# Performance work log

Hardware: AMD Instinct MI355X
Metric: run time of the kernel (lower is better)

The kernel has to match this reference:

```python
import jax, jax.numpy as jnp
import numpy as np

POS_L, DIR_L, TIME_L = 10, 4, 4
R, S, H = 2048, 128, 256


def posenc(x, L):
    # torch order: [x, sin(f0*x), cos(f0*x), sin(f1*x), cos(f1*x), ...]
    freqs = 2.0 ** jnp.arange(L, dtype=x.dtype)          # log-sampled bands
    xf = x[..., None, :] * freqs[:, None]                # [..., L, C]
    sc = jnp.stack([jnp.sin(xf), jnp.cos(xf)], axis=-2)  # [..., L, 2, C]
    return jnp.concatenate([x, sc.reshape(*x.shape[:-1], -1)], axis=-1)


def mlp(x, params):
    *hidden, last = params
    for W, b in hidden:
        x = jax.nn.relu(x @ W + b)
    W, b = last
    return x @ W + b


def compute_weights(sigma, z_vals):
    delta = jnp.concatenate(
        [z_vals[..., 1:] - z_vals[..., :-1], jnp.full_like(z_vals[..., :1], 1e10)], axis=-1)
    alpha = 1.0 - jnp.exp(-sigma * delta)
    trans = jnp.cumprod(
        jnp.concatenate([jnp.ones_like(alpha[..., :1]), 1.0 - alpha + 1e-10], axis=-1),
        axis=-1)[..., :-1]
    return alpha * trans


def _init_mlp(kbase, dims):
    Ws, bs = [], []
    for i, (din, dout) in enumerate(zip(dims[:-1], dims[1:])):
        Ws.append(jax.random.normal(jax.random.fold_in(kbase, i), (din, dout), jnp.float32)
                  / jnp.sqrt(jnp.float32(din)))
        bs.append(jnp.zeros((dout,), jnp.float32))
    bs[-1] = bs[-1].at[0].set(1.0)  # bias sigma positive so compositing is well-behaved
    return Ws, bs


def setup_inputs() -> dict:
    key = jax.random.key(0)
    k = jax.random.split(key, 6)
    points = jax.random.normal(k[0], (R, S, 3), jnp.float32)
    dirs = jax.random.normal(k[1], (R, S, 3), jnp.float32)
    z_vals = 2.0 + 4.0 * jnp.sort(jax.random.uniform(k[2], (R, S), jnp.float32), axis=-1)
    time = jax.random.uniform(k[3], (R, S), jnp.float32)
    sdims = [90, H, H, H, H, 4]
    ddims = [99, H, H, H, H, 5]
    sW, sb = _init_mlp(k[4], sdims)
    dW, db = _init_mlp(k[5], ddims)
    inp = {"points": points, "dirs": dirs, "z_vals": z_vals, "time": time}
    for i in range(5):
        inp[f"static_W{i}"] = sW[i]
        inp[f"static_b{i}"] = sb[i]
        inp[f"dynamic_W{i}"] = dW[i]
        inp[f"dynamic_b{i}"] = db[i]
    return inp


def reference(points, dirs, z_vals, time,
              static_W0, static_b0, static_W1, static_b1, static_W2, static_b2,
              static_W3, static_b3, static_W4, static_b4,
              dynamic_W0, dynamic_b0, dynamic_W1, dynamic_b1, dynamic_W2, dynamic_b2,
              dynamic_W3, dynamic_b3, dynamic_W4, dynamic_b4):
    sparams = [(static_W0, static_b0), (static_W1, static_b1), (static_W2, static_b2),
               (static_W3, static_b3), (static_W4, static_b4)]
    dparams = [(dynamic_W0, dynamic_b0), (dynamic_W1, dynamic_b1), (dynamic_W2, dynamic_b2),
               (dynamic_W3, dynamic_b3), (dynamic_W4, dynamic_b4)]

    enc_p = posenc(points, POS_L)                 # [R,S,63]
    enc_d = posenc(dirs, DIR_L)                   # [R,S,27]
    enc_t = posenc(time[..., None], TIME_L)       # [R,S,9]

    static_out = mlp(jnp.concatenate([enc_p, enc_d], axis=-1), sparams)            # [R,S,4]
    dynamic_out = mlp(jnp.concatenate([enc_p, enc_d, enc_t], axis=-1), dparams)    # [R,S,5]

    static_sigma = static_out[..., 0]
    static_rgb = jax.nn.sigmoid(static_out[..., 1:4])
    dynamic_sigma = dynamic_out[..., 0]
    dynamic_rgb = jax.nn.sigmoid(dynamic_out[..., 1:4])
    bw = jax.nn.sigmoid(dynamic_out[..., 4])      # [R,S] blend weight

    sigma = (1.0 - bw) * static_sigma + bw * dynamic_sigma           # [R,S]
    rgb = (1.0 - bw)[..., None] * static_rgb + bw[..., None] * dynamic_rgb  # [R,S,3]

    weights = compute_weights(sigma, z_vals)                         # [R,S]
    rgb_map = jnp.sum(weights[..., None] * rgb, axis=-2)             # [R,3]
    depth_map = jnp.sum(weights * z_vals, axis=-1)                   # [R]
    static_weights = (1.0 - bw) * weights
    dynamic_weights = bw * weights
    return rgb_map, depth_map, weights, static_weights, dynamic_weights
```

## Files before the change

### kernel.cpp

```cpp
#include <hip/hip_runtime.h>
#include <math.h>


#define RAYS 2048
#define SAMP 128
#define MTOT (RAYS * SAMP)
#define HD   256
#define BM   128
#define ES   136
#define HS   264

#define OUT_RGB   0
#define OUT_DEPTH 6144
#define OUT_W     8192
#define OUT_SW    270336
#define OUT_DW    532480

#define SW0 0
#define SW1 32768
#define SW2 98304
#define SW3 163840
#define SW4 229376
#define DW0 233472
#define DW1 266240
#define DW2 331776
#define DW3 397312
#define DW4 462848
#define WTOT 466944

typedef __attribute__((ext_vector_type(8))) short short8;
typedef __attribute__((ext_vector_type(4))) float f32x4;
typedef __attribute__((ext_vector_type(2))) float f32x2;
typedef __attribute__((ext_vector_type(2))) unsigned int uint2v;

__device__ __forceinline__ float sigm(float x) { return 1.0f / (1.0f + expf(-x)); }

__device__ __forceinline__ short f2bf(float f) {
    union { float f; unsigned u; } v; v.f = f;
    unsigned r = v.u + 0x7fffu + ((v.u >> 16) & 1u);
    return (short)(r >> 16);
}

#define GLB_LOAD(dst, ptr, imm) \
    asm volatile("global_load_dwordx4 %0, %1, off offset:%c2" \
                 : "=v"(dst) : "v"(ptr), "n"(imm))
#define LDS_READ(dst, addr, imm) \
    asm volatile("ds_read_b128 %0, %1 offset:%c2" \
                 : "=v"(dst) : "v"(addr), "n"(imm))
#define WAITCNT(vm, lg) do { \
    asm volatile("s_waitcnt vmcnt(%c0) lgkmcnt(%c1)" :: "n"(vm), "n"(lg)); \
    __builtin_amdgcn_sched_barrier(0); } while (0)

__device__ __forceinline__ void bar_lgkm() {
    __builtin_amdgcn_sched_barrier(0);
    asm volatile("s_waitcnt lgkmcnt(0)\n\ts_barrier" ::: "memory");
    __builtin_amdgcn_sched_barrier(0);
}
__device__ __forceinline__ void bar_only() {
    __builtin_amdgcn_sched_barrier(0);
    asm volatile("s_barrier" ::: "memory");
    __builtin_amdgcn_sched_barrier(0);
}

__device__ __forceinline__ void conv1(const float* __restrict__ src, short* __restrict__ dst,
                                      int local, int K, int N, int Kpad) {
    const int n = local / Kpad, k = local - n * Kpad;
    const float v = (k < K && n < N) ? src[k * N + n] : 0.0f;
    dst[local] = f2bf(v);
}

__global__ __launch_bounds__(256)
void prep_weights(const float* sW0, const float* sW1, const float* sW2,
                  const float* sW3, const float* sW4,
                  const float* dW0, const float* dW1, const float* dW2,
                  const float* dW3, const float* dW4, short* __restrict__ dst)
{
    const int idx = blockIdx.x * 256 + threadIdx.x;
    if (idx >= WTOT) return;
    if      (idx < SW1) conv1(sW0, dst + SW0, idx - SW0,  90, 256, 128);
    else if (idx < SW2) conv1(sW1, dst + SW1, idx - SW1, 256, 256, 256);
    else if (idx < SW3) conv1(sW2, dst + SW2, idx - SW2, 256, 256, 256);
    else if (idx < SW4) conv1(sW3, dst + SW3, idx - SW3, 256, 256, 256);
    else if (idx < DW0) conv1(sW4, dst + SW4, idx - SW4, 256,   4, 256);
    else if (idx < DW1) conv1(dW0, dst + DW0, idx - DW0,  99, 256, 128);
    else if (idx < DW2) conv1(dW1, dst + DW1, idx - DW1, 256, 256, 256);
    else if (idx < DW3) conv1(dW2, dst + DW2, idx - DW2, 256, 256, 256);
    else if (idx < DW4) conv1(dW3, dst + DW3, idx - DW3, 256, 256, 256);
    else                conv1(dW4, dst + DW4, idx - DW4, 256,   5, 256);
}

template <int KSTEPS, bool RELU, int AS, bool BAR1 = true>
__device__ __forceinline__ void layer256(const short* A,
                                         const short* __restrict__ Wt,
                                         const float* __restrict__ bias,
                                         short* O, int Os, int tid)
{
    const int w = tid >> 6, lane = tid & 63, qq = lane >> 4, col = lane & 15;
    constexpr int K = KSTEPS * 32;

    const short* wp0 = Wt + (size_t)(w * 64 +  0 + col) * K + qq * 8;
    const short* wp1 = Wt + (size_t)(w * 64 + 16 + col) * K + qq * 8;
    const short* wp2 = Wt + (size_t)(w * 64 + 32 + col) * K + qq * 8;
    const short* wp3 = Wt + (size_t)(w * 64 + 48 + col) * K + qq * 8;
    const unsigned ab = (unsigned)(size_t)(const void*)A + (unsigned)((col * AS + qq * 8) * 2);

    short8 wa[2][4], ba[2][4];

    GLB_LOAD(wa[0][0], wp0, 0);
    GLB_LOAD(wa[0][1], wp1, 0);
    GLB_LOAD(wa[0][2], wp2, 0);
    GLB_LOAD(wa[0][3], wp3, 0);
    LDS_READ(ba[0][0], ab, (0 * 16 * AS) * 2);
    LDS_READ(ba[0][1], ab, (1 * 16 * AS) * 2);
    LDS_READ(ba[0][2], ab, (2 * 16 * AS) * 2);
    LDS_READ(ba[0][3], ab, (3 * 16 * AS) * 2);

    f32x4 acc[4][8];
#pragma unroll
    for (int ft = 0; ft < 4; ft++)
#pragma unroll
        for (int st = 0; st < 8; st++) acc[ft][st] = (f32x4)0.0f;

#pragma unroll
    for (int kk = 0; kk < KSTEPS; kk++) {
        const int c = kk & 1, nx = c ^ 1;
        if (kk + 1 < KSTEPS) {
            GLB_LOAD(wa[nx][0], wp0, (kk + 1) * 64);
            GLB_LOAD(wa[nx][1], wp1, (kk + 1) * 64);
            GLB_LOAD(wa[nx][2], wp2, (kk + 1) * 64);
            GLB_LOAD(wa[nx][3], wp3, (kk + 1) * 64);
        }
        LDS_READ(ba[1][0], ab, (4 * 16 * AS) * 2 + kk * 64);
        LDS_READ(ba[1][1], ab, (5 * 16 * AS) * 2 + kk * 64);
        LDS_READ(ba[1][2], ab, (6 * 16 * AS) * 2 + kk * 64);
        LDS_READ(ba[1][3], ab, (7 * 16 * AS) * 2 + kk * 64);
        if (kk + 1 < KSTEPS) WAITCNT(4, 4);
        else                 WAITCNT(0, 4);
        __builtin_amdgcn_s_setprio(1);
#pragma unroll
        for (int ft = 0; ft < 4; ft++)
#pragma unroll
            for (int st = 0; st < 4; st++)
                acc[ft][st] = __builtin_amdgcn_mfma_f32_16x16x32_bf16(
                    wa[c][ft], ba[0][st], acc[ft][st], 0, 0, 0);
        __builtin_amdgcn_s_setprio(0);
        if (kk + 1 < KSTEPS) {
            LDS_READ(ba[0][0], ab, (0 * 16 * AS) * 2 + (kk + 1) * 64);
            LDS_READ(ba[0][1], ab, (1 * 16 * AS) * 2 + (kk + 1) * 64);
            LDS_READ(ba[0][2], ab, (2 * 16 * AS) * 2 + (kk + 1) * 64);
            LDS_READ(ba[0][3], ab, (3 * 16 * AS) * 2 + (kk + 1) * 64);
            WAITCNT(4, 4);
        } else {
            WAITCNT(0, 0);
        }
        __builtin_amdgcn_s_setprio(1);
#pragma unroll
        for (int ft = 0; ft < 4; ft++)
#pragma unroll
            for (int st = 0; st < 4; st++)
                acc[ft][4 + st] = __builtin_amdgcn_mfma_f32_16x16x32_bf16(
                    wa[c][ft], ba[1][st], acc[ft][4 + st], 0, 0, 0);
        __builtin_amdgcn_s_setprio(0);
    }

    if (BAR1) bar_only();

#pragma unroll
    for (int ft = 0; ft < 4; ft++) {
        const f32x4 bv = *(const f32x4*)(bias + w * 64 + ft * 16 + qq * 4);
#pragma unroll
        for (int st = 0; st < 8; st++) {
            float v0 = acc[ft][st][0] + bv[0];
            float v1 = acc[ft][st][1] + bv[1];
            float v2 = acc[ft][st][2] + bv[2];
            float v3 = acc[ft][st][3] + bv[3];
            if (RELU) {
                v0 = fmaxf(v0, 0.0f); v1 = fmaxf(v1, 0.0f);
                v2 = fmaxf(v2, 0.0f); v3 = fmaxf(v3, 0.0f);
            }
            unsigned p0, p1;
            asm("v_cvt_pk_bf16_f32 %0, %1, %2" : "=v"(p0) : "v"(v0), "v"(v1));
            asm("v_cvt_pk_bf16_f32 %0, %1, %2" : "=v"(p1) : "v"(v2), "v"(v3));
            uint2v pk; pk[0] = p0; pk[1] = p1;
            *(uint2v*)(O + (size_t)(st * 16 + col) * Os + w * 64 + ft * 16 + qq * 4) = pk;
        }
    }
    bar_lgkm();
}

template <int NV, int OS>
__device__ __forceinline__ void head256(const short* A, int As,
                                        const short* __restrict__ Wt,
                                        const float* __restrict__ bias,
                                        float* Out, int tid)
{
    const int w = tid >> 6, lane = tid & 63, qq = lane >> 4, col = lane & 15;
#pragma unroll
    for (int g = 0; g < 2; g++) {
        const int s = g * 64 + w * 16 + col;
        f32x4 acc = (f32x4)0.0f;
#pragma unroll
        for (int kk = 0; kk < 8; kk++) {
            short8 a = *(const short8*)(Wt + col * 256 + kk * 32 + qq * 8);
            short8 b = *(const short8*)(A + (size_t)s * As + kk * 32 + qq * 8);
            acc = __builtin_amdgcn_mfma_f32_16x16x32_bf16(a, b, acc, 0, 0, 0);
        }
        if (qq == 0) {
#pragma unroll
            for (int i = 0; i < 4; i++) Out[s * OS + i] = acc[i] + bias[i];
        } else if (NV == 5 && qq == 1) {
            Out[s * OS + 4] = acc[0] + bias[4];
        }
    }
}

__global__ __launch_bounds__(256, 1)
void nerf_mlp(const float* __restrict__ points, const float* __restrict__ dirsv,
              const float* __restrict__ timev, const short* __restrict__ wt,
              const float* __restrict__ sb0, const float* __restrict__ sb1,
              const float* __restrict__ sb2, const float* __restrict__ sb3,
              const float* __restrict__ sb4,
              const float* __restrict__ db0, const float* __restrict__ db1,
              const float* __restrict__ db2, const float* __restrict__ db3,
              const float* __restrict__ db4,
              float* __restrict__ o_sigma, float* __restrict__ o_r,
              float* __restrict__ o_g, float* __restrict__ o_b,
              float* __restrict__ o_bw)
{
    __shared__ __align__(16) short E[BM][ES];
    __shared__ __align__(16) short Hb[BM][HS];
    __shared__ float so[BM][4];
    __shared__ float dn[BM][5];

    const int tid = threadIdx.x;
    const int m0  = blockIdx.x * BM;

    for (int idx = tid; idx < 7 * BM; idx += 256) {
        const int c = idx >> 7, s = idx & 127, m = m0 + s;
        float x; int dbase, nb, dstep, coff;
        if (c < 3)      { x = points[m * 3 + c];     E[s][c]      = f2bf(x); dbase = 3 + c;  nb = 10; dstep = 6; coff = 3; }
        else if (c < 6) { x = dirsv[m * 3 + c - 3];  E[s][60 + c] = f2bf(x); dbase = 63 + c; nb = 4;  dstep = 6; coff = 3; }
        else            { x = timev[m];              E[s][90]     = f2bf(x); dbase = 91;     nb = 4;  dstep = 2; coff = 1; }
        float sl = sinf(x), cl = cosf(x);
        int d = dbase;
        E[s][d] = f2bf(sl); E[s][d + coff] = f2bf(cl);
        for (int l = 1; l < nb; l++) {
            const float s2 = 2.0f * sl * cl;
            const float c2 = cl * cl - sl * sl;
            d += dstep;
            E[s][d] = f2bf(s2); E[s][d + coff] = f2bf(c2);
            sl = s2; cl = c2;
        }
    }
    for (int idx = tid; idx < BM * 32; idx += 256) {
        const int s = idx >> 5, d = 96 + (idx & 31);
        if (d >= 99) E[s][d] = 0;
    }
    bar_lgkm();

    layer256<4, true, ES, false>(&E[0][0],  wt + SW0, sb0, &Hb[0][0], HS, tid);
    layer256<8, true, HS>(&Hb[0][0], wt + SW1, sb1, &Hb[0][0], HS, tid);
    layer256<8, true, HS>(&Hb[0][0], wt + SW2, sb2, &Hb[0][0], HS, tid);
    layer256<8, true, HS>(&Hb[0][0], wt + SW3, sb3, &Hb[0][0], HS, tid);
    head256<4, 4>(&Hb[0][0], HS, wt + SW4, sb4, &so[0][0], tid);

    layer256<4, true, ES>(&E[0][0],  wt + DW0, db0, &Hb[0][0], HS, tid);
    layer256<8, true, HS>(&Hb[0][0], wt + DW1, db1, &Hb[0][0], HS, tid);
    layer256<8, true, HS>(&Hb[0][0], wt + DW2, db2, &Hb[0][0], HS, tid);
    layer256<8, true, HS>(&Hb[0][0], wt + DW3, db3, &Hb[0][0], HS, tid);
    head256<5, 5>(&Hb[0][0], HS, wt + DW4, db4, &dn[0][0], tid);
    bar_lgkm();

    if (tid < BM) {
        const int s = tid, m = m0 + s;
        const float bw = sigm(dn[s][4]);
        const float sigma = (1.f - bw) * so[s][0] + bw * dn[s][0];
        const float r  = (1.f - bw) * sigm(so[s][1]) + bw * sigm(dn[s][1]);
        const float gg = (1.f - bw) * sigm(so[s][2]) + bw * sigm(dn[s][2]);
        const float bb = (1.f - bw) * sigm(so[s][3]) + bw * sigm(dn[s][3]);
        o_sigma[m] = sigma; o_r[m] = r; o_g[m] = gg; o_b[m] = bb; o_bw[m] = bw;
    }
}

__global__ __launch_bounds__(256)
void nerf_comp(const float* __restrict__ zv,
               const float* __restrict__ o_sigma, const float* __restrict__ o_r,
               const float* __restrict__ o_g, const float* __restrict__ o_b,
               const float* __restrict__ o_bw, float* __restrict__ out)
{
    const int ray  = blockIdx.x * 4 + (threadIdx.x >> 6);
    const int lane = threadIdx.x & 63;
    const int base = ray * SAMP;

    const f32x2 z01 = *(const f32x2*)(zv + base + 2 * lane);
    const float z0 = z01[0], z1 = z01[1];
    const float z2 = __shfl_down(z0, 1);
    const float d0 = z1 - z0;
    const float d1 = (lane < 63) ? (z2 - z1) : 1e10f;

    const f32x2 sg = *(const f32x2*)(o_sigma + base + 2 * lane);
    const float a0 = 1.0f - expf(-sg[0] * d0);
    const float a1 = 1.0f - expf(-sg[1] * d1);
    const float f0 = 1.0f - a0 + 1e-10f;
    const float f1 = 1.0f - a1 + 1e-10f;

    float incl = f0 * f1;
#pragma unroll
    for (int dlt = 1; dlt < 64; dlt <<= 1) {
        const float t = __shfl_up(incl, dlt);
        if (lane >= dlt) incl *= t;
    }
    float ex = __shfl_up(incl, 1);
    if (lane == 0) ex = 1.0f;

    const float t0 = ex;
    const float t1 = ex * f0;
    const float w0 = a0 * t0, w1 = a1 * t1;

    const f32x2 bw2 = *(const f32x2*)(o_bw + base + 2 * lane);
    f32x2 vw;  vw[0] = w0;                   vw[1] = w1;
    f32x2 vsw; vsw[0] = (1.f - bw2[0]) * w0; vsw[1] = (1.f - bw2[1]) * w1;
    f32x2 vdw; vdw[0] = bw2[0] * w0;         vdw[1] = bw2[1] * w1;
    *(f32x2*)(out + OUT_W  + base + 2 * lane) = vw;
    *(f32x2*)(out + OUT_SW + base + 2 * lane) = vsw;
    *(f32x2*)(out + OUT_DW + base + 2 * lane) = vdw;

    const f32x2 r2 = *(const f32x2*)(o_r + base + 2 * lane);
    const f32x2 g2 = *(const f32x2*)(o_g + base + 2 * lane);
    const f32x2 b2 = *(const f32x2*)(o_b + base + 2 * lane);
    float pr = w0 * r2[0] + w1 * r2[1];
    float pg = w0 * g2[0] + w1 * g2[1];
    float pb = w0 * b2[0] + w1 * b2[1];
    float pd = w0 * z0 + w1 * z1;
#pragma unroll
    for (int dlt = 32; dlt >= 1; dlt >>= 1) {
        pr += __shfl_down(pr, dlt);
        pg += __shfl_down(pg, dlt);
        pb += __shfl_down(pb, dlt);
        pd += __shfl_down(pd, dlt);
    }
    if (lane == 0) {
        out[OUT_RGB + ray * 3 + 0] = pr;
        out[OUT_RGB + ray * 3 + 1] = pg;
        out[OUT_RGB + ray * 3 + 2] = pb;
        out[OUT_DEPTH + ray] = pd;
    }
}

extern "C" void kernel_launch(void* const* d_in, const int* in_sizes, int n_in,
                              void* d_out, int out_size, void* d_ws, size_t ws_size,
                              hipStream_t stream)
{
    const float* points = (const float*)d_in[0];
    const float* dirsv  = (const float*)d_in[1];
    const float* zvals  = (const float*)d_in[2];
    const float* timev  = (const float*)d_in[3];

    const float *sW[5], *sb[5], *dW[5], *db[5];
    if (in_sizes[6] == 99 * 256) {
        for (int i = 0; i < 5; i++) {
            sW[i] = (const float*)d_in[4 + 4 * i + 0];
            sb[i] = (const float*)d_in[4 + 4 * i + 1];
            dW[i] = (const float*)d_in[4 + 4 * i + 2];
            db[i] = (const float*)d_in[4 + 4 * i + 3];
        }
    } else {
        for (int i = 0; i < 5; i++) {
            sW[i] = (const float*)d_in[4 + 2 * i + 0];
            sb[i] = (const float*)d_in[4 + 2 * i + 1];
            dW[i] = (const float*)d_in[14 + 2 * i + 0];
            db[i] = (const float*)d_in[14 + 2 * i + 1];
        }
    }

    short* wt = (short*)d_ws;
    float* ws = (float*)((char*)d_ws + (size_t)WTOT * 2);
    float* o_sigma = ws;
    float* o_r  = ws + (size_t)MTOT * 1;
    float* o_g  = ws + (size_t)MTOT * 2;
    float* o_b  = ws + (size_t)MTOT * 3;
    float* o_bw = ws + (size_t)MTOT * 4;

    prep_weights<<<(WTOT + 255) / 256, 256, 0, stream>>>(
        sW[0], sW[1], sW[2], sW[3], sW[4], dW[0], dW[1], dW[2], dW[3], dW[4], wt);

    nerf_mlp<<<MTOT / BM, 256, 0, stream>>>(points, dirsv, timev, wt,
        sb[0], sb[1], sb[2], sb[3], sb[4], db[0], db[1], db[2], db[3], db[4],
        o_sigma, o_r, o_g, o_b, o_bw);

    nerf_comp<<<RAYS / 4, 256, 0, stream>>>(zvals, o_sigma, o_r, o_g, o_b, o_bw,
                                            (float*)d_out);
}
```

Baseline: 456.1 us.

## Double row tile to 256 samples per block, reusing activation buffer for encodings

Raises the per-block sample tile from 128 to 256. Each weight fragment loaded from global memory now feeds twice as many MFMAs, which halves weight traffic per sample, and the accumulator array doubles to 64 f32x4 per thread. The separate encoding buffer is dropped: the positional encoding is written into the hidden buffer and recomputed before the dynamic MLP so LDS fits. Layers become noinline calls. The risks are much higher register pressure, half as many blocks (1024) for the GPU to schedule, extra encoding work, and call overhead.

```diff
diff --git a/kernel.cpp b/kernel.cpp
--- a/kernel.cpp
+++ b/kernel.cpp
@@ -6,8 +6,7 @@
 #define SAMP 128
 #define MTOT (RAYS * SAMP)
 #define HD   256
-#define BM   128
-#define ES   136
+#define BM   256
 #define HS   264
 
 #define OUT_RGB   0
@@ -89,20 +88,50 @@
     else                conv1(dW4, dst + DW4, idx - DW4, 256,   5, 256);
 }
 
-template <int KSTEPS, bool RELU, int AS, bool BAR1 = true>
-__device__ __forceinline__ void layer256(const short* A,
-                                         const short* __restrict__ Wt,
-                                         const float* __restrict__ bias,
-                                         short* O, int Os, int tid)
+__device__ __attribute__((noinline))
+void encode_E(short* __restrict__ Hb, const float* __restrict__ points,
+              const float* __restrict__ dirsv, const float* __restrict__ timev,
+              int m0, int tid)
+{
+    for (int idx = tid; idx < 7 * BM; idx += 256) {
+        const int c = idx >> 8, s = idx & 255, m = m0 + s;
+        short* E = Hb + (size_t)s * HS;
+        float x; int dbase, nb, dstep, coff;
+        if (c < 3)      { x = points[m * 3 + c];     E[c]      = f2bf(x); dbase = 3 + c;  nb = 10; dstep = 6; coff = 3; }
+        else if (c < 6) { x = dirsv[m * 3 + c - 3];  E[60 + c] = f2bf(x); dbase = 63 + c; nb = 4;  dstep = 6; coff = 3; }
+        else            { x = timev[m];              E[90]     = f2bf(x); dbase = 91;     nb = 4;  dstep = 2; coff = 1; }
+        float sl = sinf(x), cl = cosf(x);
+        int d = dbase;
+        E[d] = f2bf(sl); E[d + coff] = f2bf(cl);
+        for (int l = 1; l < nb; l++) {
+            const float s2 = 2.0f * sl * cl;
+            const float c2 = cl * cl - sl * sl;
+            d += dstep;
+            E[d] = f2bf(s2); E[d + coff] = f2bf(c2);
+            sl = s2; cl = c2;
+        }
+    }
+    for (int idx = tid; idx < BM * 32; idx += 256) {
+        const int s = idx >> 5, d = 96 + (idx & 31);
+        if (d >= 99) Hb[(size_t)s * HS + d] = 0;
+    }
+}
+
+template <int KSTEPS, bool RELU>
+__device__ __attribute__((noinline))
+void layer256(const short* A, const short* __restrict__ Wt,
+              const float* __restrict__ bias, short* O, int tid)
 {
     const int w = tid >> 6, lane = tid & 63, qq = lane >> 4, col = lane & 15;
     constexpr int K = KSTEPS * 32;
+    constexpr int NPH = 4 * KSTEPS;
 
     const short* wp0 = Wt + (size_t)(w * 64 +  0 + col) * K + qq * 8;
     const short* wp1 = Wt + (size_t)(w * 64 + 16 + col) * K + qq * 8;
     const short* wp2 = Wt + (size_t)(w * 64 + 32 + col) * K + qq * 8;
     const short* wp3 = Wt + (size_t)(w * 64 + 48 + col) * K + qq * 8;
-    const unsigned ab = (unsigned)(size_t)(const void*)A + (unsigned)((col * AS + qq * 8) * 2);
+    const unsigned ab  = (unsigned)(size_t)(const void*)A + (unsigned)((col * HS + qq * 8) * 2);
+    const unsigned abH = ab + 8 * 16 * HS * 2;
 
     short8 wa[2][4], ba[2][4];
 
@@ -110,66 +139,53 @@
     GLB_LOAD(wa[0][1], wp1, 0);
     GLB_LOAD(wa[0][2], wp2, 0);
     GLB_LOAD(wa[0][3], wp3, 0);
-    LDS_READ(ba[0][0], ab, (0 * 16 * AS) * 2);
-    LDS_READ(ba[0][1], ab, (1 * 16 * AS) * 2);
-    LDS_READ(ba[0][2], ab, (2 * 16 * AS) * 2);
-    LDS_READ(ba[0][3], ab, (3 * 16 * AS) * 2);
-
-    f32x4 acc[4][8];
+    LDS_READ(ba[0][0], ab, (0 * 16 * HS) * 2);
+    LDS_READ(ba[0][1], ab, (1 * 16 * HS) * 2);
+    LDS_READ(ba[0][2], ab, (2 * 16 * HS) * 2);
+    LDS_READ(ba[0][3], ab, (3 * 16 * HS) * 2);
+
+    f32x4 acc[4][16];
 #pragma unroll
     for (int ft = 0; ft < 4; ft++)
 #pragma unroll
-        for (int st = 0; st < 8; st++) acc[ft][st] = (f32x4)0.0f;
-
-#pragma unroll
-    for (int kk = 0; kk < KSTEPS; kk++) {
-        const int c = kk & 1, nx = c ^ 1;
-        if (kk + 1 < KSTEPS) {
-            GLB_LOAD(wa[nx][0], wp0, (kk + 1) * 64);
-            GLB_LOAD(wa[nx][1], wp1, (kk + 1) * 64);
-            GLB_LOAD(wa[nx][2], wp2, (kk + 1) * 64);
-            GLB_LOAD(wa[nx][3], wp3, (kk + 1) * 64);
-        }
-        LDS_READ(ba[1][0], ab, (4 * 16 * AS) * 2 + kk * 64);
-        LDS_READ(ba[1][1], ab, (5 * 16 * AS) * 2 + kk * 64);
-        LDS_READ(ba[1][2], ab, (6 * 16 * AS) * 2 + kk * 64);
-        LDS_READ(ba[1][3], ab, (7 * 16 * AS) * 2 + kk * 64);
-        if (kk + 1 < KSTEPS) WAITCNT(4, 4);
-        else                 WAITCNT(0, 4);
+        for (int st = 0; st < 16; st++) acc[ft][st] = (f32x4)0.0f;
+
+#pragma unroll
+    for (int P = 0; P < NPH; P++) {
+        const int kk = P >> 2, q = P & 3, ca = P & 1, cw = kk & 1;
+        if (q == 0 && kk + 1 < KSTEPS) {
+            GLB_LOAD(wa[cw ^ 1][0], wp0, (kk + 1) * 64);
+            GLB_LOAD(wa[cw ^ 1][1], wp1, (kk + 1) * 64);
+            GLB_LOAD(wa[cw ^ 1][2], wp2, (kk + 1) * 64);
+            GLB_LOAD(wa[cw ^ 1][3], wp3, (kk + 1) * 64);
+        }
+        if (P + 1 < NPH) {
+            const int nP = P + 1, nkk = nP >> 2, nq = nP & 3, na = nP & 1;
+            LDS_READ(ba[na][0], (nq < 2 ? ab : abH), (((nq * 4 + 0) & 7) * 16 * HS) * 2 + nkk * 64);
+            LDS_READ(ba[na][1], (nq < 2 ? ab : abH), (((nq * 4 + 1) & 7) * 16 * HS) * 2 + nkk * 64);
+            LDS_READ(ba[na][2], (nq < 2 ? ab : abH), (((nq * 4 + 2) & 7) * 16 * HS) * 2 + nkk * 64);
+            LDS_READ(ba[na][3], (nq < 2 ? ab : abH), (((nq * 4 + 3) & 7) * 16 * HS) * 2 + nkk * 64);
+        }
+        if (kk + 1 < KSTEPS) { WAITCNT(4, 4); }
+        else if (P + 1 < NPH) { WAITCNT(0, 4); }
+        else                  { WAITCNT(0, 0); }
         __builtin_amdgcn_s_setprio(1);
 #pragma unroll
         for (int ft = 0; ft < 4; ft++)
 #pragma unroll
             for (int st = 0; st < 4; st++)
-                acc[ft][st] = __builtin_amdgcn_mfma_f32_16x16x32_bf16(
-                    wa[c][ft], ba[0][st], acc[ft][st], 0, 0, 0);
+                acc[ft][q * 4 + st] = __builtin_amdgcn_mfma_f32_16x16x32_bf16(
+                    wa[cw][ft], ba[ca][st], acc[ft][q * 4 + st], 0, 0, 0);
         __builtin_amdgcn_s_setprio(0);
-        if (kk + 1 < KSTEPS) {
-            LDS_READ(ba[0][0], ab, (0 * 16 * AS) * 2 + (kk + 1) * 64);
-            LDS_READ(ba[0][1], ab, (1 * 16 * AS) * 2 + (kk + 1) * 64);
-            LDS_READ(ba[0][2], ab, (2 * 16 * AS) * 2 + (kk + 1) * 64);
-            LDS_READ(ba[0][3], ab, (3 * 16 * AS) * 2 + (kk + 1) * 64);
-            WAITCNT(4, 4);
-        } else {
-            WAITCNT(0, 0);
-        }
-        __builtin_amdgcn_s_setprio(1);
-#pragma unroll
-        for (int ft = 0; ft < 4; ft++)
-#pragma unroll
-            for (int st = 0; st < 4; st++)
-                acc[ft][4 + st] = __builtin_amdgcn_mfma_f32_16x16x32_bf16(
-                    wa[c][ft], ba[1][st], acc[ft][4 + st], 0, 0, 0);
-        __builtin_amdgcn_s_setprio(0);
-    }
-
-    if (BAR1) bar_only();
+    }
+
+    bar_only();
 
 #pragma unroll
     for (int ft = 0; ft < 4; ft++) {
         const f32x4 bv = *(const f32x4*)(bias + w * 64 + ft * 16 + qq * 4);
 #pragma unroll
-        for (int st = 0; st < 8; st++) {
+        for (int st = 0; st < 16; st++) {
             float v0 = acc[ft][st][0] + bv[0];
             float v1 = acc[ft][st][1] + bv[1];
             float v2 = acc[ft][st][2] + bv[2];
@@ -182,27 +198,26 @@
             asm("v_cvt_pk_bf16_f32 %0, %1, %2" : "=v"(p0) : "v"(v0), "v"(v1));
             asm("v_cvt_pk_bf16_f32 %0, %1, %2" : "=v"(p1) : "v"(v2), "v"(v3));
             uint2v pk; pk[0] = p0; pk[1] = p1;
-            *(uint2v*)(O + (size_t)(st * 16 + col) * Os + w * 64 + ft * 16 + qq * 4) = pk;
+            *(uint2v*)(O + (size_t)(st * 16 + col) * HS + w * 64 + ft * 16 + qq * 4) = pk;
         }
     }
     bar_lgkm();
 }
 
 template <int NV, int OS>
-__device__ __forceinline__ void head256(const short* A, int As,
-                                        const short* __restrict__ Wt,
+__device__ __forceinline__ void head256(const short* A, const short* __restrict__ Wt,
                                         const float* __restrict__ bias,
                                         float* Out, int tid)
 {
     const int w = tid >> 6, lane = tid & 63, qq = lane >> 4, col = lane & 15;
 #pragma unroll
-    for (int g = 0; g < 2; g++) {
+    for (int g = 0; g < 4; g++) {
         const int s = g * 64 + w * 16 + col;
         f32x4 acc = (f32x4)0.0f;
 #pragma unroll
         for (int kk = 0; kk < 8; kk++) {
             short8 a = *(const short8*)(Wt + col * 256 + kk * 32 + qq * 8);
-            short8 b = *(const short8*)(A + (size_t)s * As + kk * 32 + qq * 8);
+            short8 b = *(const short8*)(A + (size_t)s * HS + kk * 32 + qq * 8);
             acc = __builtin_amdgcn_mfma_f32_16x16x32_bf16(a, b, acc, 0, 0, 0);
         }
         if (qq == 0) {
@@ -227,7 +242,6 @@
               float* __restrict__ o_g, float* __restrict__ o_b,
               float* __restrict__ o_bw)
 {
-    __shared__ __align__(16) short E[BM][ES];
     __shared__ __align__(16) short Hb[BM][HS];
     __shared__ float so[BM][4];
     __shared__ float dn[BM][5];
@@ -235,43 +249,26 @@
     const int tid = threadIdx.x;
     const int m0  = blockIdx.x * BM;
 
-    for (int idx = tid; idx < 7 * BM; idx += 256) {
-        const int c = idx >> 7, s = idx & 127, m = m0 + s;
-        float x; int dbase, nb, dstep, coff;
-        if (c < 3)      { x = points[m * 3 + c];     E[s][c]      = f2bf(x); dbase = 3 + c;  nb = 10; dstep = 6; coff = 3; }
-        else if (c < 6) { x = dirsv[m * 3 + c - 3];  E[s][60 + c] = f2bf(x); dbase = 63 + c; nb = 4;  dstep = 6; coff = 3; }
-        else            { x = timev[m];              E[s][90]     = f2bf(x); dbase = 91;     nb = 4;  dstep = 2; coff = 1; }
-        float sl = sinf(x), cl = cosf(x);
-        int d = dbase;
-        E[s][d] = f2bf(sl); E[s][d + coff] = f2bf(cl);
-        for (int l = 1; l < nb; l++) {
-            const float s2 = 2.0f * sl * cl;
-            const float c2 = cl * cl - sl * sl;
-            d += dstep;
-            E[s][d] = f2bf(s2); E[s][d + coff] = f2bf(c2);
-            sl = s2; cl = c2;
-        }
-    }
-    for (int idx = tid; idx < BM * 32; idx += 256) {
-        const int s = idx >> 5, d = 96 + (idx & 31);
-        if (d >= 99) E[s][d] = 0;
-    }
+    encode_E(&Hb[0][0], points, dirsv, timev, m0, tid);
     bar_lgkm();
 
-    layer256<4, true, ES, false>(&E[0][0],  wt + SW0, sb0, &Hb[0][0], HS, tid);
-    layer256<8, true, HS>(&Hb[0][0], wt + SW1, sb1, &Hb[0][0], HS, tid);
-    layer256<8, true, HS>(&Hb[0][0], wt + SW2, sb2, &Hb[0][0], HS, tid);
-    layer256<8, true, HS>(&Hb[0][0], wt + SW3, sb3, &Hb[0][0], HS, tid);
-    head256<4, 4>(&Hb[0][0], HS, wt + SW4, sb4, &so[0][0], tid);
-
-    layer256<4, true, ES>(&E[0][0],  wt + DW0, db0, &Hb[0][0], HS, tid);
-    layer256<8, true, HS>(&Hb[0][0], wt + DW1, db1, &Hb[0][0], HS, tid);
-    layer256<8, true, HS>(&Hb[0][0], wt + DW2, db2, &Hb[0][0], HS, tid);
-    layer256<8, true, HS>(&Hb[0][0], wt + DW3, db3, &Hb[0][0], HS, tid);
-    head256<5, 5>(&Hb[0][0], HS, wt + DW4, db4, &dn[0][0], tid);
+    layer256<4, true>(&Hb[0][0], wt + SW0, sb0, &Hb[0][0], tid);
+    layer256<8, true>(&Hb[0][0], wt + SW1, sb1, &Hb[0][0], tid);
+    layer256<8, true>(&Hb[0][0], wt + SW2, sb2, &Hb[0][0], tid);
+    layer256<8, true>(&Hb[0][0], wt + SW3, sb3, &Hb[0][0], tid);
+    head256<4, 4>(&Hb[0][0], wt + SW4, sb4, &so[0][0], tid);
+    bar_only();
+
+    encode_E(&Hb[0][0], points, dirsv, timev, m0, tid);
     bar_lgkm();
-
-    if (tid < BM) {
+    layer256<4, true>(&Hb[0][0], wt + DW0, db0, &Hb[0][0], tid);
+    layer256<8, true>(&Hb[0][0], wt + DW1, db1, &Hb[0][0], tid);
+    layer256<8, true>(&Hb[0][0], wt + DW2, db2, &Hb[0][0], tid);
+    layer256<8, true>(&Hb[0][0], wt + DW3, db3, &Hb[0][0], tid);
+    head256<5, 5>(&Hb[0][0], wt + DW4, db4, &dn[0][0], tid);
+    bar_lgkm();
+
+    {
         const int s = tid, m = m0 + s;
         const float bw = sigm(dn[s][4]);
         const float sigma = (1.f - bw) * so[s][0] + bw * dn[s][0];
```

Measured after the change: 686.5 us. 50.5% more time.
